# Performance work log

Measured on AMD Instinct MI355X. Metric: run time of the kernel, lower is better.

Reference implementation:

```python
import jax, jax.numpy as jnp
import numpy as np

NUM_GRAPHS = 64
NODES_PER_GRAPH = 256
EDGES_PER_GRAPH = 1024
D_FEAT = 512
H_FIL = 1024
H_PHI = 256
N_CLASSES = 10


def _xavier(k, fan_in, fan_out):
    s = float(np.sqrt(6.0 / (fan_in + fan_out)))
    return jax.random.uniform(k, (fan_in, fan_out), jnp.float32, -s, s)


def setup_inputs() -> dict:
    key = jax.random.key(0)
    ks = jax.random.split(key, 8)
    N = NUM_GRAPHS * NODES_PER_GRAPH
    x = jax.random.normal(ks[0], (N, D_FEAT), jnp.float32)
    # per-graph local edge endpoints, offset to global vertex ids
    el = jax.random.randint(ks[1], (NUM_GRAPHS, EDGES_PER_GRAPH, 2), 0, NODES_PER_GRAPH)
    offs = (jnp.arange(NUM_GRAPHS) * NODES_PER_GRAPH)[:, None, None]
    edges = (el + offs).reshape(-1, 2).astype(jnp.int32)
    sample_id = jnp.repeat(jnp.arange(NUM_GRAPHS, dtype=jnp.int32), NODES_PER_GRAPH)
    return {
        "x": x,
        "edges": edges,
        "sample_id": sample_id,
        "w_fil1": _xavier(ks[2], D_FEAT, H_FIL),
        "b_fil1": jnp.full((H_FIL,), 0.01, jnp.float32),
        "w_fil2": _xavier(ks[3], H_FIL, 1),
        "b_fil2": jnp.full((1,), 0.01, jnp.float32),
        "w_phi0": _xavier(ks[4], 2, H_PHI),
        "b_phi0": jnp.full((H_PHI,), 0.01, jnp.float32),
        "w_phi1": _xavier(ks[5], 2, H_PHI),
        "b_phi1": jnp.full((H_PHI,), 0.01, jnp.float32),
        "w_head": _xavier(ks[6], 2 * H_PHI, N_CLASSES),
        "b_head": jnp.full((N_CLASSES,), 0.01, jnp.float32),
    }


def vertex_persistence_deaths(f, edges):
    """0-dim sublevel-set persistence of a vertex filtration via union-find.

    Returns death value per vertex (birth is f[v]):
      - vertices killed by an edge merge (elder rule) die at max(f_u, f_v);
      - per-component survivors (essential classes) are paired with the
        max filtration value of their component (extended persistence).
    Pairing indices are discrete; death VALUES stay differentiable w.r.t. f.
    """
    N = f.shape[0]
    w = jnp.maximum(f[edges[:, 0]], f[edges[:, 1]])
    order = jnp.argsort(w)  # process edges in increasing filtration order
    eu, ev, ew = edges[order, 0], edges[order, 1], w[order]

    def find(parent, u):
        return jax.lax.while_loop(lambda r: parent[r] != r, lambda r: parent[r], u)

    def body(carry, uvw):
        parent, death, paired = carry
        u, v, wv = uvw
        ru = find(parent, u)
        rv = find(parent, v)
        # path compression of the two endpoints
        parent = parent.at[u].set(ru).at[v].set(rv)
        u_elder = (f[ru] < f[rv]) | ((f[ru] == f[rv]) & (ru < rv))
        elder = jnp.where(u_elder, ru, rv)
        young = jnp.where(u_elder, rv, ru)
        merge = ru != rv
        parent = parent.at[young].set(jnp.where(merge, elder, parent[young]))
        death = death.at[young].set(jnp.where(merge, wv, death[young]))
        paired = paired.at[young].set(paired[young] | merge)
        return (parent, death, paired), None

    init = (jnp.arange(N, dtype=eu.dtype), jnp.zeros(N, f.dtype), jnp.zeros(N, bool))
    (parent, death, paired), _ = jax.lax.scan(body, init, (eu, ev, ew))
    # full path compression by repeated pointer jumping (integer-only)
    parent = jax.lax.while_loop(lambda p: jnp.any(p[p] != p), lambda p: p[p], parent)
    comp_max = jnp.full((N,), -jnp.inf, f.dtype).at[parent].max(f)
    return jnp.where(paired, death, comp_max[parent])


def reference(x, edges, sample_id, w_fil1, b_fil1, w_fil2, b_fil2,
              w_phi0, b_phi0, w_phi1, b_phi1, w_head, b_head):
    # fil: node filtration in (0, 1)
    h = jax.nn.relu(x @ w_fil1 + b_fil1)
    f = jax.nn.sigmoid(h @ w_fil2 + b_fil2)[:, 0]  # [N]

    # sublevel persistence -> h0 pairs (birth, death), one per vertex
    d_sub = vertex_persistence_deaths(f, edges)
    h0 = jnp.stack([f, d_sub], axis=1)  # [N, 2]

    # superlevel persistence via -f, then negate & swap -> h1 pairs
    d_sup = vertex_persistence_deaths(-f, edges)
    h1 = jnp.stack([-d_sup, f], axis=1)  # (-death_sup, -birth_sup) = (-d_sup, f)

    # cls: per-pair MLP + sum pooling per graph, linear head
    phi0 = jax.nn.relu(h0 @ w_phi0 + b_phi0)  # [N, H_PHI]
    phi1 = jax.nn.relu(h1 @ w_phi1 + b_phi1)
    p0 = jax.ops.segment_sum(phi0, sample_id, num_segments=NUM_GRAPHS)
    p1 = jax.ops.segment_sum(phi1, sample_id, num_segments=NUM_GRAPHS)
    feats = jnp.concatenate([p0, p1], axis=1)  # [B, 2*H_PHI]
    return feats @ w_head + b_head  # [B, N_CLASSES]
```

## Files before the change

kernel.cpp:

```cpp
#include <hip/hip_runtime.h>
#include <hip/hip_bf16.h>

#define NUM_GRAPHS 64
#define NODES 256
#define EDGES 1024
#define NTOT (NUM_GRAPHS * NODES)
#define DF 512
#define HF 1024
#define HP 256
#define NC 10
#define INF32 0xFFFFFFFFu

typedef short bf16x8 __attribute__((ext_vector_type(8)));
typedef float f32x4 __attribute__((ext_vector_type(4)));

__device__ __forceinline__ unsigned short bf16r(float f) {
    __hip_bfloat16 h = __float2bfloat16(f);
    return *(unsigned short*)&h;
}
__device__ __forceinline__ unsigned encf(float x) {
    union { float f; unsigned u; } c; c.f = x;
    return (c.u & 0x80000000u) ? ~c.u : (c.u | 0x80000000u);
}

__global__ __launch_bounds__(256) void k_cvt_frag(
    const float* __restrict__ w1, unsigned short* __restrict__ w1f)
{
    __shared__ float ls[128 * 16];
    const int tid = threadIdx.x;
    const int cg = blockIdx.x >> 2, kq = blockIdx.x & 3;
    const int c = tid & 15, kr = tid >> 4;
#pragma unroll
    for (int it = 0; it < 8; ++it) {
        int kk = it * 16 + kr;
        ls[kk * 16 + c] = w1[(size_t)(kq * 128 + kk) * HF + cg * 16 + c];
    }
    __syncthreads();
    const int tt = tid >> 6, n16 = tid & 15, q = (tid >> 4) & 3;
    unsigned short v[8];
#pragma unroll
    for (int j = 0; j < 8; ++j)
        v[j] = bf16r(ls[(tt * 32 + q * 8 + j) * 16 + n16]);
    size_t off = ((size_t)(cg * 16 + kq * 4 + tt) * 64 + (q * 16 + n16)) * 8;
#pragma unroll
    for (int j = 0; j < 8; ++j) w1f[off + j] = v[j];
}

__global__ __launch_bounds__(256, 1) void k_fil_mfma(
    const float* __restrict__ x, const unsigned short* __restrict__ w1f,
    const float* __restrict__ b1, const float* __restrict__ w2,
    float* __restrict__ zbuf )
{
    __shared__ unsigned short Bbuf[4 * 16 * 512];
    __shared__ float zpart[4][32];
    const int tid = threadIdx.x;
    const int lane = tid & 63;
    const int wv = tid >> 6;
    const int l15 = lane & 15, quad = lane >> 4;
    const int half = wv >> 1;
    const int rt = wv & 1;
    const int r0 = (blockIdx.x >> 1) * 64;
    const int ch = blockIdx.x & 1;
    const int cg0 = ch * 32;
    const int rowA = r0 + rt * 32 + l15;
    const int rowB = rowA + 16;

    bf16x8 A0[16], A1[16];
#pragma unroll
    for (int t = 0; t < 16; ++t) {
        const float* s0 = x + (size_t)rowA * DF + t * 32 + quad * 8;
        const float* s1 = x + (size_t)rowB * DF + t * 32 + quad * 8;
        float4 a = *(const float4*)s0, b = *(const float4*)(s0 + 4);
        float4 c = *(const float4*)s1, d = *(const float4*)(s1 + 4);
        A0[t][0]=(short)bf16r(a.x); A0[t][1]=(short)bf16r(a.y);
        A0[t][2]=(short)bf16r(a.z); A0[t][3]=(short)bf16r(a.w);
        A0[t][4]=(short)bf16r(b.x); A0[t][5]=(short)bf16r(b.y);
        A0[t][6]=(short)bf16r(b.z); A0[t][7]=(short)bf16r(b.w);
        A1[t][0]=(short)bf16r(c.x); A1[t][1]=(short)bf16r(c.y);
        A1[t][2]=(short)bf16r(c.z); A1[t][3]=(short)bf16r(c.w);
        A1[t][4]=(short)bf16r(d.x); A1[t][5]=(short)bf16r(d.y);
        A1[t][6]=(short)bf16r(d.z); A1[t][7]=(short)bf16r(d.w);
    }

    const int t128 = tid & 127;
    const int sh = tid >> 7;
    uint4 pf[8];
    {
        const uint4* s = (const uint4*)(w1f + (size_t)(cg0 + sh * 16) * 8192);
#pragma unroll
        for (int j = 0; j < 8; ++j) pf[j] = s[t128 + j * 128];
        uint4* d = (uint4*)Bbuf + (sh * 2 + 0) * 1024;
#pragma unroll
        for (int j = 0; j < 8; ++j) d[t128 + j * 128] = pf[j];
    }
    __syncthreads();

    float s_[2][4] = {{0,0,0,0},{0,0,0,0}};

    for (int i = 0; i < 16; ++i) {
        const int par = i & 1;
        if (i < 15) {
            const uint4* s = (const uint4*)(w1f + (size_t)(cg0 + sh * 16 + i + 1) * 8192);
#pragma unroll
            for (int j = 0; j < 8; ++j) pf[j] = s[t128 + j * 128];
        }
        const unsigned short* bb = Bbuf + (half * 2 + par) * 8192 + lane * 8;
        f32x4 a00={0,0,0,0}, a01={0,0,0,0}, a10={0,0,0,0}, a11={0,0,0,0};
#pragma unroll
        for (int t = 0; t < 8; ++t) {
            bf16x8 Bf0 = *(const bf16x8*)(bb + t * 512);
            bf16x8 Bf1 = *(const bf16x8*)(bb + (t + 8) * 512);
            a00 = __builtin_amdgcn_mfma_f32_16x16x32_bf16(A0[t], Bf0, a00, 0, 0, 0);
            a10 = __builtin_amdgcn_mfma_f32_16x16x32_bf16(A1[t], Bf0, a10, 0, 0, 0);
            a01 = __builtin_amdgcn_mfma_f32_16x16x32_bf16(A0[t + 8], Bf1, a01, 0, 0, 0);
            a11 = __builtin_amdgcn_mfma_f32_16x16x32_bf16(A1[t + 8], Bf1, a11, 0, 0, 0);
        }
        const int col = (cg0 + half * 16 + i) * 16 + l15;
        const float b1c = b1[col], w2c = w2[col];
#pragma unroll
        for (int r = 0; r < 4; ++r) {
            float h0 = (a00[r] + a01[r]) + b1c; h0 = h0 > 0.f ? h0 : 0.f;
            s_[0][r] = fmaf(h0, w2c, s_[0][r]);
            float h1 = (a10[r] + a11[r]) + b1c; h1 = h1 > 0.f ? h1 : 0.f;
            s_[1][r] = fmaf(h1, w2c, s_[1][r]);
        }
        if (i < 15) {
            uint4* d = (uint4*)Bbuf + (sh * 2 + (par ^ 1)) * 1024;
#pragma unroll
            for (int j = 0; j < 8; ++j) d[t128 + j * 128] = pf[j];
        }
        __syncthreads();
    }

#pragma unroll
    for (int sub = 0; sub < 2; ++sub)
#pragma unroll
        for (int r = 0; r < 4; ++r) {
            float v = s_[sub][r];
            v += __shfl_xor(v, 1, 16);
            v += __shfl_xor(v, 2, 16);
            v += __shfl_xor(v, 4, 16);
            v += __shfl_xor(v, 8, 16);
            if (l15 == 0) zpart[wv][sub * 16 + quad * 4 + r] = v;
        }
    __syncthreads();
    if (tid < 64) {
        int rrt = tid >> 5, idx = tid & 31;
        zbuf[(size_t)ch * NTOT + r0 + tid] = zpart[rrt][idx] + zpart[rrt + 2][idx];
    }
}

#define TN2 16
__global__ __launch_bounds__(256) void k_fil(
    const float* __restrict__ x, const float* __restrict__ w1,
    const float* __restrict__ b1, const float* __restrict__ w2,
    float* __restrict__ zout)
{
    __shared__ float xs[TN2][DF];
    __shared__ float part[256];
    const int tid = threadIdx.x;
    const int n0 = blockIdx.x * TN2;
    for (int c = tid; c < TN2 * DF / 4; c += 256) {
        int n = c >> 7, k4 = (c & 127) << 2;
        *(float4*)&xs[n][k4] = *(const float4*)(x + (size_t)(n0 + n) * DF + k4);
    }
    __syncthreads();
    float h[TN2][4];
#pragma unroll
    for (int n = 0; n < TN2; ++n)
#pragma unroll
        for (int q = 0; q < 4; ++q) h[n][q] = 0.f;
    for (int k = 0; k < DF; ++k) {
        float wr[4];
#pragma unroll
        for (int q = 0; q < 4; ++q) wr[q] = w1[(size_t)k * HF + tid + 256 * q];
#pragma unroll
        for (int n = 0; n < TN2; ++n) {
            float xv = xs[n][k];
#pragma unroll
            for (int q = 0; q < 4; ++q) h[n][q] = fmaf(xv, wr[q], h[n][q]);
        }
    }
    float b1r[4], w2r[4];
#pragma unroll
    for (int q = 0; q < 4; ++q) { b1r[q] = b1[tid + 256 * q]; w2r[q] = w2[tid + 256 * q]; }
    for (int n = 0; n < TN2; ++n) {
        float s = 0.f;
#pragma unroll
        for (int q = 0; q < 4; ++q) {
            float hv = h[n][q] + b1r[q];
            s += (hv > 0.f ? hv : 0.f) * w2r[q];
        }
        part[tid] = s;
        __syncthreads();
        for (int off = 128; off > 0; off >>= 1) {
            if (tid < off) part[tid] += part[tid + off];
            __syncthreads();
        }
        if (tid == 0) zout[n0 + n] = part[0];
        __syncthreads();
    }
}

__global__ __launch_bounds__(512) void k_pers(
    const int* __restrict__ edges, const float* __restrict__ zbuf,
    const float* __restrict__ b2, float* __restrict__ dout )
{
    const int bid = blockIdx.x;
    const int g = bid >> 1, sgn = bid & 1;
    const int tid = threadIdx.x;
    const int v = tid & 255, vh = tid >> 8;

    __shared__ float fv[NODES];
    __shared__ __align__(16) unsigned long long vkey[NODES];
    __shared__ int order_[NODES], rank_[NODES];
    __shared__ float fvr[NODES];
    __shared__ unsigned eks[EDGES];
    __shared__ int comp[NODES];
    __shared__ unsigned minE[NODES];
    __shared__ int nxt[NODES], par2[NODES];
    __shared__ unsigned char mstflag[EDGES];
    __shared__ int cnt, chg;
    __shared__ __align__(16) unsigned mstK[NODES];
    __shared__ unsigned srt[NODES];
    __shared__ int dr[NODES + 64];
    __shared__ int cmaxr[NODES];
    __shared__ int rkp[512];

    if (tid < 256) {
        float z0 = zbuf[g * NODES + tid] + zbuf[NTOT + g * NODES + tid];
        float f0 = 1.f / (1.f + expf(-(z0 + b2[0])));
        fv[tid] = sgn ? -f0 : f0;
        vkey[tid] = ((unsigned long long)encf(fv[tid]) << 32) | (unsigned)tid;
        srt[tid] = INF32; dr[tid] = 0; cmaxr[tid] = 0;
        comp[tid] = tid;
    }
    __syncthreads();

    {
        const unsigned long long mk = vkey[v];
        const int j0 = vh << 7;
        int c = 0;
#pragma unroll 8
        for (int j = j0; j < j0 + 128; j += 2) {
            ulonglong2 kk = *(const ulonglong2*)&vkey[j];
            c += (kk.x < mk) ? 1 : 0;
            c += (kk.y < mk) ? 1 : 0;
        }
        rkp[tid] = c;
    }
    __syncthreads();
    if (tid < 256) {
        int rk = rkp[tid] + rkp[tid + 256];
        order_[rk] = tid;
        rank_[tid] = rk;
        fvr[rk] = fv[tid];
    }
    __syncthreads();

#pragma unroll
    for (int q = 0; q < 2; ++q) {
        int e = tid + q * 512;
        int u = edges[2 * (g * EDGES + e)]     - g * NODES;
        int w = edges[2 * (g * EDGES + e) + 1] - g * NODES;
        if (u == w) { eks[e] = INF32; }
        else {
            int ra = rank_[u], rb = rank_[w];
            int rlo = ra < rb ? ra : rb, rhi = ra < rb ? rb : ra;
            eks[e] = ((unsigned)rhi << 18) | ((unsigned)e << 8) | (unsigned)rlo;
        }
        mstflag[e] = 0;
    }
    __syncthreads();

    for (int round = 0; round < 8; ++round) {
        if (tid < 256) minE[tid] = INF32;
        if (tid == 0) chg = 0;
        __syncthreads();
#pragma unroll
        for (int q = 0; q < 2; ++q) {
            int e = tid + q * 512;
            unsigned k = eks[e];
            if (k != INF32) {
                int rlo = (int)(k & 255u), rhi = (int)(k >> 18);
                int cu = comp[rlo], cv = comp[rhi];
                if (cu != cv) {
                    atomicMin(&minE[cu], k);
                    atomicMin(&minE[cv], k);
                } else if (!mstflag[e]) {
                    eks[e] = INF32;
                }
            }
        }
        __syncthreads();
        if (tid < 256) {
            unsigned mk = minE[tid];
            int o = tid;
            if (mk != INF32) {
                int rlo = (int)(mk & 255u), rhi = (int)(mk >> 18);
                int cu = comp[rlo], cv = comp[rhi];
                o = (cu == tid) ? cv : cu;
                mstflag[(mk >> 8) & 0x3FFu] = 1;
                chg = 1;
            }
            nxt[tid] = o;
        }
        __syncthreads();
        if (!chg) break;
        if (tid < 256) {
            int o = nxt[tid];
            int p = o;
            if (nxt[o] == tid && tid < o) p = tid;
            par2[tid] = p;
        }
        __syncthreads();
        for (;;) {
            int p = par2[par2[v]];
            int done = __syncthreads_and(p == par2[v]);
            if (done) break;
            par2[v] = p;
            __syncthreads();
        }
        if (tid < 256) comp[tid] = par2[comp[tid]];
        __syncthreads();
        if (__syncthreads_and(comp[v] == comp[0])) break;
    }

    if (tid == 0) cnt = 0;
    __syncthreads();
#pragma unroll
    for (int q = 0; q < 2; ++q) {
        int e = tid + q * 512;
        if (mstflag[e]) {
            int p = atomicAdd(&cnt, 1);
            mstK[p] = eks[e];
        }
    }
    __syncthreads();
    if (tid < 256 && tid >= cnt) mstK[tid] = INF32;
    __syncthreads();

    {
        const unsigned m2 = mstK[v];
        const int j0 = vh << 7;
        int c = 0;
        if (m2 != INF32) {
#pragma unroll 8
            for (int j = j0; j < j0 + 128; j += 4) {
                uint4 kk = *(const uint4*)&mstK[j];
                c += (kk.x < m2) ? 1 : 0;
                c += (kk.y < m2) ? 1 : 0;
                c += (kk.z < m2) ? 1 : 0;
                c += (kk.w < m2) ? 1 : 0;
            }
        }
        rkp[tid] = c;
    }
    __syncthreads();
    if (tid < 256) {
        unsigned m2 = mstK[tid];
        if (m2 != INF32) srt[rkp[tid] + rkp[tid + 256]] = m2;
    }
    __syncthreads();

    if (tid < 64) {
        const int ln = tid;
        unsigned rpack = (unsigned)ln * 0x01010101u + 0xC0804000u;
        int sv0 = (int)srt[ln], sv1 = (int)srt[ln + 64];
        int sv2 = (int)srt[ln + 128], sv3 = (int)srt[ln + 192];
        const int n = cnt;
        for (int blk = 0; blk < 4; ++blk) {
            const int base = blk << 6;
            if (base >= n) break;
            int lim = n - base; if (lim > 64) lim = 64;
            const int svb = blk == 0 ? sv0 : blk == 1 ? sv1 : blk == 2 ? sv2 : sv3;
            for (int sl = 0; sl < lim; ++sl) {
                const unsigned k = (unsigned)__builtin_amdgcn_readlane(svb, sl);
                const int lo = (int)(k & 255u);
                const int hi = (int)((k >> 18) & 255u);
                const unsigned va = (unsigned)__builtin_amdgcn_readlane((int)rpack, lo & 63);
                const int ca = (int)((va >> ((lo >> 6) << 3)) & 255u);
                const unsigned vb = (unsigned)__builtin_amdgcn_readlane((int)rpack, hi & 63);
                const int cb = (int)((vb >> ((hi >> 6) << 3)) & 255u);
                const int elder = ca < cb ? ca : cb;
                const int young = ca > cb ? ca : cb;
                const unsigned y4 = (unsigned)young * 0x01010101u;
                const unsigned d4 = (unsigned)(young ^ elder) * 0x01010101u;
                const unsigned mm = rpack ^ y4;
                const unsigned ww = (mm | 0x80808080u) - 0x01010101u;
                const unsigned zm = ~(ww | mm) & 0x80808080u;
                rpack ^= d4 & ((zm >> 7) * 255u);
                dr[(ln == 0) ? young : (NODES + ln)] = hi;
            }
        }
    }
    __syncthreads();

    if (tid < 256) {
        atomicMax(&cmaxr[comp[tid]], tid);
    }
    __syncthreads();

    if (tid < 256) {
        const int db = dr[tid];
        float dv = (db != 0) ? fvr[db] : fvr[cmaxr[comp[tid]]];
        dout[sgn * NTOT + g * NODES + order_[tid]] = dv;
    }
}

__global__ __launch_bounds__(256) void k_head(
    const float* __restrict__ zbuf, const float* __restrict__ b2,
    const float* __restrict__ dbuf,
    const float* __restrict__ wp0, const float* __restrict__ bp0,
    const float* __restrict__ wp1, const float* __restrict__ bp1,
    const float* __restrict__ wh, const float* __restrict__ bh,
    float* __restrict__ out)
{
    const int g = blockIdx.x, tid = threadIdx.x;
    const int lane = tid & 63, wv = tid >> 6;
    __shared__ float lf[NODES], l0[NODES], l1[NODES];
    __shared__ float wpart[4][NC];
    {
        float z0 = zbuf[g * NODES + tid] + zbuf[NTOT + g * NODES + tid];
        lf[tid] = 1.f / (1.f + expf(-(z0 + b2[0])));
    }
    l0[tid] = dbuf[g * NODES + tid];
    l1[tid] = dbuf[NTOT + g * NODES + tid];
    __syncthreads();
    const float w00 = wp0[tid], w01 = wp0[HP + tid], bb0 = bp0[tid];
    const float w10 = wp1[tid], w11 = wp1[HP + tid], bb1 = bp1[tid];
    float s0 = 0.f, s1 = 0.f;
    for (int n = 0; n < NODES; ++n) {
        float f = lf[n], d0 = l0[n], d1 = l1[n];
        float a0 = fmaf(f, w00, fmaf(d0, w01, bb0));
        float a1 = fmaf(-d1, w10, fmaf(f, w11, bb1));
        s0 += a0 > 0.f ? a0 : 0.f;
        s1 += a1 > 0.f ? a1 : 0.f;
    }
    float pc[NC];
    const float* whr0 = wh + (size_t)tid * NC;
    const float* whr1 = wh + (size_t)(HP + tid) * NC;
#pragma unroll
    for (int c = 0; c < NC; ++c) pc[c] = s0 * whr0[c] + s1 * whr1[c];
#pragma unroll
    for (int off = 32; off > 0; off >>= 1)
#pragma unroll
        for (int c = 0; c < NC; ++c) pc[c] += __shfl_xor(pc[c], off, 64);
    if (lane == 0)
#pragma unroll
        for (int c = 0; c < NC; ++c) wpart[wv][c] = pc[c];
    __syncthreads();
    if (tid < NC)
        out[g * NC + tid] = bh[tid] + wpart[0][tid] + wpart[1][tid]
                          + wpart[2][tid] + wpart[3][tid];
}

extern "C" void kernel_launch(void* const* d_in, const int* in_sizes, int n_in,
                              void* d_out, int out_size, void* d_ws, size_t ws_size,
                              hipStream_t stream)
{
    const float* x   = (const float*)d_in[0];
    const int*   edg = (const int*)d_in[1];
    const float* w1  = (const float*)d_in[3];
    const float* b1  = (const float*)d_in[4];
    const float* w2  = (const float*)d_in[5];
    const float* b2  = (const float*)d_in[6];
    const float* wp0 = (const float*)d_in[7];
    const float* bp0 = (const float*)d_in[8];
    const float* wp1 = (const float*)d_in[9];
    const float* bp1 = (const float*)d_in[10];
    const float* wh  = (const float*)d_in[11];
    const float* bh  = (const float*)d_in[12];

    float* zbuf = (float*)d_ws;
    float* dbuf = zbuf + 2 * NTOT;
    unsigned short* w1f = (unsigned short*)(dbuf + 2 * NTOT);

    const size_t WS_REQ = (size_t)4 * NTOT * 4 + (size_t)HF * DF * 2 + 256;

    if (ws_size >= WS_REQ) {
        k_cvt_frag<<<256, 256, 0, stream>>>(w1, w1f);
        k_fil_mfma<<<512, 256, 0, stream>>>(x, w1f, b1, w2, zbuf);
    } else {
        hipMemsetAsync(zbuf + NTOT, 0, (size_t)NTOT * 4, stream);
        k_fil     <<<NTOT / TN2, 256, 0, stream>>>(x, w1, b1, w2, zbuf);
    }
    k_pers<<<NUM_GRAPHS * 2, 512, 0, stream>>>(edg, zbuf, b2, dbuf);
    k_head<<<NUM_GRAPHS, 256, 0, stream>>>(zbuf, b2, dbuf, wp0, bp0, wp1, bp1,
                                           wh, bh, (float*)d_out);
}
```

Baseline: 174.3 us.

## Split fil GEMM into four column-quarter blocks with lighter per-wave work

The MFMA filtration kernel is reorganised so each block covers 64 rows and a quarter of the hidden columns. Each wave now owns 16 rows with a single accumulator, which halves the A-fragment registers and shrinks LDS. That allows up to 4 blocks per CU, and 1024 blocks are launched instead of 512. Partial z sums go to four buffers that the downstream kernels add together. The cost is reloading each x row four times across blocks and fewer MFMAs per B-tile LDS read, which gives less reuse per block.

```diff
diff --git a/kernel.cpp b/kernel.cpp
--- a/kernel.cpp
+++ b/kernel.cpp
@@ -46,108 +46,85 @@
     for (int j = 0; j < 8; ++j) w1f[off + j] = v[j];
 }
 
-__global__ __launch_bounds__(256, 1) void k_fil_mfma(
+__global__ __launch_bounds__(256, 4) void k_fil_mfma(
     const float* __restrict__ x, const unsigned short* __restrict__ w1f,
     const float* __restrict__ b1, const float* __restrict__ w2,
     float* __restrict__ zbuf )
 {
-    __shared__ unsigned short Bbuf[4 * 16 * 512];
-    __shared__ float zpart[4][32];
+    __shared__ unsigned short Bbuf[2 * 8192];
+    __shared__ float zpart[4][16];
     const int tid = threadIdx.x;
     const int lane = tid & 63;
     const int wv = tid >> 6;
     const int l15 = lane & 15, quad = lane >> 4;
-    const int half = wv >> 1;
-    const int rt = wv & 1;
-    const int r0 = (blockIdx.x >> 1) * 64;
-    const int ch = blockIdx.x & 1;
-    const int cg0 = ch * 32;
-    const int rowA = r0 + rt * 32 + l15;
-    const int rowB = rowA + 16;
-
-    bf16x8 A0[16], A1[16];
+    const int r0 = (blockIdx.x >> 2) * 64;
+    const int cq = blockIdx.x & 3;
+    const int cg0 = cq * 16;
+    const int row = r0 + wv * 16 + l15;
+
+    bf16x8 A[16];
 #pragma unroll
     for (int t = 0; t < 16; ++t) {
-        const float* s0 = x + (size_t)rowA * DF + t * 32 + quad * 8;
-        const float* s1 = x + (size_t)rowB * DF + t * 32 + quad * 8;
+        const float* s0 = x + (size_t)row * DF + t * 32 + quad * 8;
         float4 a = *(const float4*)s0, b = *(const float4*)(s0 + 4);
-        float4 c = *(const float4*)s1, d = *(const float4*)(s1 + 4);
-        A0[t][0]=(short)bf16r(a.x); A0[t][1]=(short)bf16r(a.y);
-        A0[t][2]=(short)bf16r(a.z); A0[t][3]=(short)bf16r(a.w);
-        A0[t][4]=(short)bf16r(b.x); A0[t][5]=(short)bf16r(b.y);
-        A0[t][6]=(short)bf16r(b.z); A0[t][7]=(short)bf16r(b.w);
-        A1[t][0]=(short)bf16r(c.x); A1[t][1]=(short)bf16r(c.y);
-        A1[t][2]=(short)bf16r(c.z); A1[t][3]=(short)bf16r(c.w);
-        A1[t][4]=(short)bf16r(d.x); A1[t][5]=(short)bf16r(d.y);
-        A1[t][6]=(short)bf16r(d.z); A1[t][7]=(short)bf16r(d.w);
-    }
-
-    const int t128 = tid & 127;
-    const int sh = tid >> 7;
-    uint4 pf[8];
+        A[t][0]=(short)bf16r(a.x); A[t][1]=(short)bf16r(a.y);
+        A[t][2]=(short)bf16r(a.z); A[t][3]=(short)bf16r(a.w);
+        A[t][4]=(short)bf16r(b.x); A[t][5]=(short)bf16r(b.y);
+        A[t][6]=(short)bf16r(b.z); A[t][7]=(short)bf16r(b.w);
+    }
+
     {
-        const uint4* s = (const uint4*)(w1f + (size_t)(cg0 + sh * 16) * 8192);
-#pragma unroll
-        for (int j = 0; j < 8; ++j) pf[j] = s[t128 + j * 128];
-        uint4* d = (uint4*)Bbuf + (sh * 2 + 0) * 1024;
-#pragma unroll
-        for (int j = 0; j < 8; ++j) d[t128 + j * 128] = pf[j];
-    }
-    __syncthreads();
-
-    float s_[2][4] = {{0,0,0,0},{0,0,0,0}};
+        const uint4* s = (const uint4*)(w1f + (size_t)cg0 * 8192);
+        uint4* d = (uint4*)Bbuf;
+#pragma unroll
+        for (int j = 0; j < 4; ++j) d[tid + j * 256] = s[tid + j * 256];
+    }
+    __syncthreads();
+
+    float s_[4] = {0, 0, 0, 0};
 
     for (int i = 0; i < 16; ++i) {
         const int par = i & 1;
+        uint4 pf[4];
         if (i < 15) {
-            const uint4* s = (const uint4*)(w1f + (size_t)(cg0 + sh * 16 + i + 1) * 8192);
-#pragma unroll
-            for (int j = 0; j < 8; ++j) pf[j] = s[t128 + j * 128];
-        }
-        const unsigned short* bb = Bbuf + (half * 2 + par) * 8192 + lane * 8;
-        f32x4 a00={0,0,0,0}, a01={0,0,0,0}, a10={0,0,0,0}, a11={0,0,0,0};
-#pragma unroll
-        for (int t = 0; t < 8; ++t) {
-            bf16x8 Bf0 = *(const bf16x8*)(bb + t * 512);
-            bf16x8 Bf1 = *(const bf16x8*)(bb + (t + 8) * 512);
-            a00 = __builtin_amdgcn_mfma_f32_16x16x32_bf16(A0[t], Bf0, a00, 0, 0, 0);
-            a10 = __builtin_amdgcn_mfma_f32_16x16x32_bf16(A1[t], Bf0, a10, 0, 0, 0);
-            a01 = __builtin_amdgcn_mfma_f32_16x16x32_bf16(A0[t + 8], Bf1, a01, 0, 0, 0);
-            a11 = __builtin_amdgcn_mfma_f32_16x16x32_bf16(A1[t + 8], Bf1, a11, 0, 0, 0);
-        }
-        const int col = (cg0 + half * 16 + i) * 16 + l15;
+            const uint4* s = (const uint4*)(w1f + (size_t)(cg0 + i + 1) * 8192);
+#pragma unroll
+            for (int j = 0; j < 4; ++j) pf[j] = s[tid + j * 256];
+        }
+        const unsigned short* bb = Bbuf + par * 8192 + lane * 8;
+        f32x4 a0 = {0, 0, 0, 0};
+#pragma unroll
+        for (int t = 0; t < 16; ++t) {
+            bf16x8 Bf = *(const bf16x8*)(bb + t * 512);
+            a0 = __builtin_amdgcn_mfma_f32_16x16x32_bf16(A[t], Bf, a0, 0, 0, 0);
+        }
+        const int col = (cg0 + i) * 16 + l15;
         const float b1c = b1[col], w2c = w2[col];
 #pragma unroll
         for (int r = 0; r < 4; ++r) {
-            float h0 = (a00[r] + a01[r]) + b1c; h0 = h0 > 0.f ? h0 : 0.f;
-            s_[0][r] = fmaf(h0, w2c, s_[0][r]);
-            float h1 = (a10[r] + a11[r]) + b1c; h1 = h1 > 0.f ? h1 : 0.f;
-            s_[1][r] = fmaf(h1, w2c, s_[1][r]);
+            float h0 = a0[r] + b1c; h0 = h0 > 0.f ? h0 : 0.f;
+            s_[r] = fmaf(h0, w2c, s_[r]);
         }
         if (i < 15) {
-            uint4* d = (uint4*)Bbuf + (sh * 2 + (par ^ 1)) * 1024;
-#pragma unroll
-            for (int j = 0; j < 8; ++j) d[t128 + j * 128] = pf[j];
-        }
-        __syncthreads();
-    }
-
-#pragma unroll
-    for (int sub = 0; sub < 2; ++sub)
-#pragma unroll
-        for (int r = 0; r < 4; ++r) {
-            float v = s_[sub][r];
-            v += __shfl_xor(v, 1, 16);
-            v += __shfl_xor(v, 2, 16);
-            v += __shfl_xor(v, 4, 16);
-            v += __shfl_xor(v, 8, 16);
-            if (l15 == 0) zpart[wv][sub * 16 + quad * 4 + r] = v;
-        }
-    __syncthreads();
-    if (tid < 64) {
-        int rrt = tid >> 5, idx = tid & 31;
-        zbuf[(size_t)ch * NTOT + r0 + tid] = zpart[rrt][idx] + zpart[rrt + 2][idx];
-    }
+            uint4* d = (uint4*)Bbuf + (par ^ 1) * 1024;
+#pragma unroll
+            for (int j = 0; j < 4; ++j) d[tid + j * 256] = pf[j];
+        }
+        __syncthreads();
+    }
+
+#pragma unroll
+    for (int r = 0; r < 4; ++r) {
+        float vv = s_[r];
+        vv += __shfl_xor(vv, 1, 16);
+        vv += __shfl_xor(vv, 2, 16);
+        vv += __shfl_xor(vv, 4, 16);
+        vv += __shfl_xor(vv, 8, 16);
+        if (l15 == 0) zpart[wv][quad * 4 + r] = vv;
+    }
+    __syncthreads();
+    if (tid < 64)
+        zbuf[(size_t)cq * NTOT + r0 + tid] = zpart[tid >> 4][tid & 15];
 }
 
 #define TN2 16
@@ -228,7 +205,8 @@
     __shared__ int rkp[512];
 
     if (tid < 256) {
-        float z0 = zbuf[g * NODES + tid] + zbuf[NTOT + g * NODES + tid];
+        float z0 = zbuf[g * NODES + tid] + zbuf[NTOT + g * NODES + tid]
+                 + zbuf[2 * NTOT + g * NODES + tid] + zbuf[3 * NTOT + g * NODES + tid];
         float f0 = 1.f / (1.f + expf(-(z0 + b2[0])));
         fv[tid] = sgn ? -f0 : f0;
         vkey[tid] = ((unsigned long long)encf(fv[tid]) << 32) | (unsigned)tid;
@@ -421,7 +399,8 @@
     __shared__ float lf[NODES], l0[NODES], l1[NODES];
     __shared__ float wpart[4][NC];
     {
-        float z0 = zbuf[g * NODES + tid] + zbuf[NTOT + g * NODES + tid];
+        float z0 = zbuf[g * NODES + tid] + zbuf[NTOT + g * NODES + tid]
+                 + zbuf[2 * NTOT + g * NODES + tid] + zbuf[3 * NTOT + g * NODES + tid];
         lf[tid] = 1.f / (1.f + expf(-(z0 + b2[0])));
     }
     l0[tid] = dbuf[g * NODES + tid];
@@ -473,16 +452,16 @@
     const float* bh  = (const float*)d_in[12];
 
     float* zbuf = (float*)d_ws;
-    float* dbuf = zbuf + 2 * NTOT;
+    float* dbuf = zbuf + 4 * NTOT;
     unsigned short* w1f = (unsigned short*)(dbuf + 2 * NTOT);
 
-    const size_t WS_REQ = (size_t)4 * NTOT * 4 + (size_t)HF * DF * 2 + 256;
+    const size_t WS_REQ = (size_t)6 * NTOT * 4 + (size_t)HF * DF * 2 + 256;
 
     if (ws_size >= WS_REQ) {
         k_cvt_frag<<<256, 256, 0, stream>>>(w1, w1f);
-        k_fil_mfma<<<512, 256, 0, stream>>>(x, w1f, b1, w2, zbuf);
+        k_fil_mfma<<<1024, 256, 0, stream>>>(x, w1f, b1, w2, zbuf);
     } else {
-        hipMemsetAsync(zbuf + NTOT, 0, (size_t)NTOT * 4, stream);
+        hipMemsetAsync(zbuf + NTOT, 0, (size_t)3 * NTOT * 4, stream);
         k_fil     <<<NTOT / TN2, 256, 0, stream>>>(x, w1, b1, w2, zbuf);
     }
     k_pers<<<NUM_GRAPHS * 2, 512, 0, stream>>>(edg, zbuf, b2, dbuf);
```

Measured after the change: 175.0 us. No clear change (+0.4%).
